# Kernel optimization log

Hardware: AMD Instinct MI355X
Metric: run time of the kernel (lower is better)

Reference implementation:

```python
import jax, jax.numpy as jnp
import numpy as np

N = 262144
K = 4  # Kernel_Correlation k
EPS = 1e-5


def setup_inputs() -> dict:
    key = jax.random.key(0)
    ks = jax.random.split(key, 12)
    inp = {
        "corner": jax.random.normal(ks[0], (N, 9), jnp.float32),
        "normal": jax.random.normal(ks[1], (N, 3), jnp.float32),
        "neighbour": jax.random.randint(ks[2], (N, 3), 0, N, jnp.int64),
        # Conv1d(1,32,6) on a length-6 signal == linear [32,6] (+bias)
        "conv_w": jax.random.normal(ks[3], (32, 6), jnp.float32) * 0.2,
        "conv_b": jax.random.normal(ks[4], (32,), jnp.float32) * 0.1,
        "lin3_w": jax.random.normal(ks[5], (64, 32), jnp.float32) * 0.15,
        "lin3_b": jnp.zeros((64,), jnp.float32),
        "lin4_w": jax.random.normal(ks[6], (64, 64), jnp.float32) * 0.12,
        "lin4_b": jnp.zeros((64,), jnp.float32),
        "kernel": jax.random.normal(ks[7], (64, K, 3), jnp.float32),  # learnable RBF kernel
        # 1x1 Conv1d(131,131) == linear [131,131]
        "conv1_w": jax.random.normal(ks[8], (131, 131), jnp.float32) * 0.08,
        "conv1_b": jnp.zeros((131,), jnp.float32),
        "bn_g": jnp.ones((131,), jnp.float32),
        "bn_b": jnp.zeros((131,), jnp.float32),
        "conv2_w": jax.random.normal(ks[9], (131, 131), jnp.float32) * 0.08,
        "conv2_b": jnp.zeros((131,), jnp.float32),
    }
    return inp


def reference(corner, normal, neighbour, conv_w, conv_b, lin3_w, lin3_b,
              lin4_w, lin4_b, kernel, conv1_w, conv1_b, bn_g, bn_b,
              conv2_w, conv2_b):
    # ---- Face_Rotate_Conv (vectorized over all n faces) ----
    c1, c2, c3 = corner[:, 0:3], corner[:, 3:6], corner[:, 6:9]
    # three rotated corner pairs: [n, 3, 6]
    pairs = jnp.stack([jnp.concatenate([c1, c2], 1),
                       jnp.concatenate([c2, c3], 1),
                       jnp.concatenate([c3, c1], 1)], axis=1)
    conv = jnp.einsum('npd,od->npo', pairs, conv_w) + conv_b  # [n,3,32]
    v = conv.mean(axis=1)                                      # [n,32]
    v = jax.nn.relu(v @ lin3_w.T + lin3_b) @ lin4_w.T + lin4_b  # [n,64]

    # ---- Kernel_Correlation (neighbour indices are gathered but unused
    # in the original math; only normal_i enters the RBF) ----
    # ||n_i - kernel_{m,l}||^2 via expansion; sq: [n,64,K]
    sq = (jnp.sum(normal * normal, 1)[:, None, None]
          + jnp.sum(kernel * kernel, -1)[None]
          - 2.0 * jnp.einsum('nd,mld->nml', normal, kernel))
    # original: sum_l exp(-norm^2) / (2*sigma^2), sigma=1, then / (k*4)
    z = jnp.sum(jnp.exp(-sq), axis=-1) * (0.5 / (K * 4))       # [n,64]

    # ---- structural_Des head ----
    x = jnp.concatenate([normal, v, z], axis=1)                # [n,131]
    h = x @ conv1_w.T + conv1_b
    # BatchNorm1d(131) in training mode: stats over the n dim (L=1)
    mean = h.mean(axis=0)
    var = jnp.mean((h - mean) ** 2, axis=0)
    h = bn_g * (h - mean) * jax.lax.rsqrt(var + EPS) + bn_b
    h = jax.nn.relu(h)
    out = h @ conv2_w.T + conv2_b                              # [n,131]
    return out
```

## Files before the change

kernel.cpp:

```cpp
#include <hip/hip_runtime.h>

#define NROWS 262144
#define NBLK  1024
#define PLANE_B   8388608ull
#define PLANE_US  4194304ull

typedef short  short8 __attribute__((ext_vector_type(8)));
typedef float  f32x4  __attribute__((ext_vector_type(4)));

static __device__ __forceinline__ unsigned short f2bf(float f) {
    unsigned u = __float_as_uint(f);
    u = u + 0x7fffu + ((u >> 16) & 1u);
    return (unsigned short)(u >> 16);
}
static __device__ __forceinline__ float bf2f(unsigned short h) {
    return __uint_as_float(((unsigned)h) << 16);
}

__global__ __launch_bounds__(256) void k_A1(
    const float* __restrict__ corner, const float* __restrict__ normal,
    const float* __restrict__ conv_w, const float* __restrict__ conv_b,
    const float* __restrict__ lin3_w, const float* __restrict__ lin3_b,
    const float* __restrict__ lin4_w, const float* __restrict__ lin4_b,
    const float* __restrict__ kern,
    unsigned short* __restrict__ X)
{
    __shared__ unsigned short T[4 * 64 * 72];
    __shared__ unsigned short B1[64 * 72];
    __shared__ unsigned short mini[4 * 64 * 20];

    const int tid  = threadIdx.x;
    const int wave = tid >> 6, lane = tid & 63;
    const int kg   = lane >> 4, c15 = lane & 15;
    const int row  = blockIdx.x * 256 + tid;

    for (int idx = tid; idx < 4096; idx += 256) {
        int o = idx >> 6, i3 = idx & 63;
        B1[o * 72 + i3] = f2bf(lin4_w[idx]);
    }

    float cr[9];
    #pragma unroll
    for (int k = 0; k < 9; k++) cr[k] = corner[row * 9 + k];
    const float nr0 = normal[row * 3 + 0];
    const float nr1 = normal[row * 3 + 1];
    const float nr2 = normal[row * 3 + 2];
    const float m0 = (cr[0] + cr[3] + cr[6]) * (1.0f / 3.0f);
    const float m1 = (cr[1] + cr[4] + cr[7]) * (1.0f / 3.0f);
    const float m2 = (cr[2] + cr[5] + cr[8]) * (1.0f / 3.0f);

    float a[32];
    #pragma unroll
    for (int o = 0; o < 32; o++) {
        const float* w = conv_w + o * 6;
        a[o] = conv_b[o] + m0 * (w[0] + w[3]) + m1 * (w[1] + w[4]) + m2 * (w[2] + w[5]);
    }

    #pragma unroll 2
    for (int i3 = 0; i3 < 64; i3++) {
        const float* w = lin3_w + i3 * 32;
        float t0 = lin3_b[i3], t1 = 0.0f;
        #pragma unroll
        for (int i = 0; i < 32; i += 2) { t0 += a[i] * w[i]; t1 += a[i + 1] * w[i + 1]; }
        float t = fmaxf(t0 + t1, 0.0f);
        T[(wave * 64 + lane) * 72 + i3] = f2bf(t);
    }

    #pragma unroll 1
    for (int cz = 0; cz < 4; cz++) {
        unsigned pk[8];
        #pragma unroll
        for (int q = 0; q < 8; q++) {
            float zz[2];
            #pragma unroll
            for (int h = 0; h < 2; h++) {
                int mi = cz * 16 + q * 2 + h;
                float acc = 0.0f;
                #pragma unroll
                for (int l = 0; l < 4; l++) {
                    const float* kp = kern + (mi * 4 + l) * 3;
                    float d0 = nr0 - kp[0], d1 = nr1 - kp[1], d2 = nr2 - kp[2];
                    acc += __expf(-(d0 * d0 + d1 * d1 + d2 * d2));
                }
                zz[h] = acc * 0.03125f;
            }
            pk[q] = (unsigned)f2bf(zz[0]) | ((unsigned)f2bf(zz[1]) << 16);
        }
        uint4* dst = (uint4*)((char*)X + (4 + cz) * PLANE_B + (size_t)row * 32);
        dst[0] = make_uint4(pk[0], pk[1], pk[2], pk[3]);
        dst[1] = make_uint4(pk[4], pk[5], pk[6], pk[7]);
    }

    __syncthreads();

    #pragma unroll 1
    for (int n = 0; n < 4; n++) {
        short8 bf0 = *(const short8*)&B1[(n * 16 + c15) * 72 + kg * 8];
        short8 bf1 = *(const short8*)&B1[(n * 16 + c15) * 72 + 32 + kg * 8];
        float bias = lin4_b[n * 16 + c15];
        #pragma unroll
        for (int m = 0; m < 4; m++) {
            f32x4 acc = {bias, bias, bias, bias};
            short8 a0 = *(const short8*)&T[(wave * 64 + m * 16 + c15) * 72 + kg * 8];
            short8 a1 = *(const short8*)&T[(wave * 64 + m * 16 + c15) * 72 + 32 + kg * 8];
            acc = __builtin_amdgcn_mfma_f32_16x16x32_bf16(a0, bf0, acc, 0, 0, 0);
            acc = __builtin_amdgcn_mfma_f32_16x16x32_bf16(a1, bf1, acc, 0, 0, 0);
            #pragma unroll
            for (int r = 0; r < 4; r++)
                mini[(wave * 64 + m * 16 + kg * 4 + r) * 20 + c15] = f2bf(acc[r]);
        }
        asm volatile("s_waitcnt lgkmcnt(0)" ::: "memory");
        const uint2* q = (const uint2*)&mini[(wave * 64 + lane) * 20];
        uint2 q0 = q[0], q1 = q[1], q2 = q[2], q3 = q[3];
        uint4* dst = (uint4*)((char*)X + (size_t)n * PLANE_B +
                              (size_t)(blockIdx.x * 256 + wave * 64 + lane) * 32);
        dst[0] = make_uint4(q0.x, q0.y, q1.x, q1.y);
        dst[1] = make_uint4(q2.x, q2.y, q3.x, q3.y);
    }
}

__global__ __launch_bounds__(256) void k_A2(
    const unsigned short* __restrict__ X, const float* __restrict__ normal,
    const float* __restrict__ w1, const float* __restrict__ b1,
    unsigned short* __restrict__ H, float* __restrict__ sums)
{
    __shared__ unsigned short Bs[144 * 168];
    __shared__ unsigned short mini[4 * 32 * 20];
    __shared__ float sl[288];

    const int tid  = threadIdx.x;
    const int wave = tid >> 6, lane = tid & 63;
    const int kg   = lane >> 4, c15 = lane & 15;

    for (int i = tid; i < 12096; i += 256) ((unsigned*)Bs)[i] = 0u;
    for (int i = tid; i < 288; i += 256) sl[i] = 0.0f;
    __syncthreads();
    for (int idx = tid; idx < 17161; idx += 256) {
        unsigned n = (unsigned)idx / 131u, ks = (unsigned)idx - n * 131u;
        unsigned kp = ks < 3 ? 128 + ks : ks - 3;
        Bs[n * 168 + kp] = f2bf(w1[idx]);
    }
    __syncthreads();

    const int rwave = blockIdx.x * 256 + wave * 64;

    #pragma unroll 1
    for (int mp = 0; mp < 2; mp++) {
        short8 af[2][5];
        #pragma unroll
        for (int mi = 0; mi < 2; mi++) {
            int arow = rwave + mp * 32 + mi * 16 + c15;
            #pragma unroll
            for (int ks = 0; ks < 4; ks++) {
                int p = ks * 2 + (kg >> 1);
                af[mi][ks] = *(const short8*)(X + (size_t)p * PLANE_US +
                                              (size_t)arow * 16 + (kg & 1) * 8);
            }
            short8 a4 = {0, 0, 0, 0, 0, 0, 0, 0};
            if (kg == 0) {
                a4[0] = (short)f2bf(normal[arow * 3 + 0]);
                a4[1] = (short)f2bf(normal[arow * 3 + 1]);
                a4[2] = (short)f2bf(normal[arow * 3 + 2]);
            }
            af[mi][4] = a4;
        }
        #pragma unroll 1
        for (int n = 0; n < 9; n++) {
            int col = n * 16 + c15;
            float bias = (col < 131) ? b1[col] : 0.0f;
            short8 bf[5];
            #pragma unroll
            for (int ks = 0; ks < 5; ks++)
                bf[ks] = *(const short8*)&Bs[(unsigned)(n * 16 + c15) * 168 + ks * 32 + kg * 8];
            f32x4 acc0 = {bias, bias, bias, bias};
            f32x4 acc1 = {bias, bias, bias, bias};
            #pragma unroll
            for (int ks = 0; ks < 5; ks++) {
                acc0 = __builtin_amdgcn_mfma_f32_16x16x32_bf16(af[0][ks], bf[ks], acc0, 0, 0, 0);
                acc1 = __builtin_amdgcn_mfma_f32_16x16x32_bf16(af[1][ks], bf[ks], acc1, 0, 0, 0);
            }
            float s1 = acc0[0] + acc0[1] + acc0[2] + acc0[3]
                     + acc1[0] + acc1[1] + acc1[2] + acc1[3];
            float s2 = acc0[0]*acc0[0] + acc0[1]*acc0[1] + acc0[2]*acc0[2] + acc0[3]*acc0[3]
                     + acc1[0]*acc1[0] + acc1[1]*acc1[1] + acc1[2]*acc1[2] + acc1[3]*acc1[3];
            s1 += __shfl_xor(s1, 16); s2 += __shfl_xor(s2, 16);
            s1 += __shfl_xor(s1, 32); s2 += __shfl_xor(s2, 32);
            if (lane < 16) { atomicAdd(&sl[col], s1); atomicAdd(&sl[144 + col], s2); }
            #pragma unroll
            for (int r = 0; r < 4; r++) {
                mini[(wave * 32 + kg * 4 + r) * 20 + c15]      = f2bf(acc0[r]);
                mini[(wave * 32 + 16 + kg * 4 + r) * 20 + c15] = f2bf(acc1[r]);
            }
            asm volatile("s_waitcnt lgkmcnt(0)" ::: "memory");
            if (lane < 32) {
                const uint2* q = (const uint2*)&mini[(wave * 32 + lane) * 20];
                uint2 q0 = q[0], q1 = q[1], q2 = q[2], q3 = q[3];
                uint4* dst = (uint4*)((char*)H + (size_t)n * PLANE_B +
                                      (size_t)(rwave + mp * 32 + lane) * 32);
                dst[0] = make_uint4(q0.x, q0.y, q1.x, q1.y);
                dst[1] = make_uint4(q2.x, q2.y, q3.x, q3.y);
            }
        }
    }
    __syncthreads();
    if (tid < 144) {
        float* dst = sums + (blockIdx.x & 63) * 288;
        atomicAdd(&dst[tid], sl[tid]);
        atomicAdd(&dst[144 + tid], sl[144 + tid]);
    }
}

__global__ void k_stats(const float* __restrict__ sums,
                        const float* __restrict__ bn_g, const float* __restrict__ bn_b,
                        float* __restrict__ scalep, float* __restrict__ shiftp)
{
    int j = threadIdx.x;
    if (j < 160) {
        float sc = 0.0f, sh = 0.0f;
        if (j < 131) {
            float s1 = 0.0f, s2 = 0.0f;
            #pragma unroll 4
            for (int s = 0; s < 64; s++) {
                s1 += sums[s * 288 + j];
                s2 += sums[s * 288 + 144 + j];
            }
            const float inv = 1.0f / (float)NROWS;
            float mean = s1 * inv;
            float var = fmaxf(s2 * inv - mean * mean, 0.0f);
            sc = bn_g[j] * rsqrtf(var + 1e-5f);
            sh = bn_b[j] - mean * sc;
        }
        scalep[j] = sc; shiftp[j] = sh;
    }
}

__global__ __launch_bounds__(256) void k_B(
    const unsigned short* __restrict__ H, const float* __restrict__ scalep,
    const float* __restrict__ shiftp, const float* __restrict__ w2,
    const float* __restrict__ b2, float* __restrict__ out)
{
    __shared__ unsigned short Bs[144 * 168];

    const int tid  = threadIdx.x;
    const int wave = tid >> 6, lane = tid & 63;
    const int kg   = lane >> 4, c15 = lane & 15;

    for (int i = tid; i < 12096; i += 256) ((unsigned*)Bs)[i] = 0u;
    __syncthreads();
    for (int idx = tid; idx < 17161; idx += 256) {
        unsigned n = (unsigned)idx / 131u, k = (unsigned)idx - n * 131u;
        Bs[n * 168 + k] = f2bf(w2[idx]);
    }
    __syncthreads();

    const int rwave = blockIdx.x * 256 + wave * 64;

    #pragma unroll 1
    for (int mp = 0; mp < 2; mp++) {
        short8 af[2][5];
        #pragma unroll
        for (int mi = 0; mi < 2; mi++) {
            int arow = rwave + mp * 32 + mi * 16 + c15;
            #pragma unroll
            for (int ks = 0; ks < 5; ks++) {
                short8 res = {0, 0, 0, 0, 0, 0, 0, 0};
                if (ks < 4 || kg < 2) {
                    int p = (ks < 4) ? (ks * 2 + (kg >> 1)) : 8;
                    short8 h8 = *(const short8*)(H + (size_t)p * PLANE_US +
                                                 (size_t)arow * 16 + (kg & 1) * 8);
                    int c0 = ks * 32 + kg * 8;
                    f32x4 scA = *(const f32x4*)(scalep + c0);
                    f32x4 scB = *(const f32x4*)(scalep + c0 + 4);
                    f32x4 shA = *(const f32x4*)(shiftp + c0);
                    f32x4 shB = *(const f32x4*)(shiftp + c0 + 4);
                    #pragma unroll
                    for (int e = 0; e < 8; e++) {
                        float hf = bf2f((unsigned short)h8[e]);
                        float sc = (e < 4) ? scA[e & 3] : scB[e & 3];
                        float sh = (e < 4) ? shA[e & 3] : shB[e & 3];
                        res[e] = (short)f2bf(fmaxf(hf * sc + sh, 0.0f));
                    }
                }
                af[mi][ks] = res;
            }
        }
        #pragma unroll 1
        for (int n = 0; n < 9; n++) {
            int col = n * 16 + c15;
            float bias = (col < 131) ? b2[col] : 0.0f;
            short8 bf[5];
            #pragma unroll
            for (int ks = 0; ks < 5; ks++)
                bf[ks] = *(const short8*)&Bs[(unsigned)(n * 16 + c15) * 168 + ks * 32 + kg * 8];
            f32x4 acc0 = {bias, bias, bias, bias};
            f32x4 acc1 = {bias, bias, bias, bias};
            #pragma unroll
            for (int ks = 0; ks < 5; ks++) {
                acc0 = __builtin_amdgcn_mfma_f32_16x16x32_bf16(af[0][ks], bf[ks], acc0, 0, 0, 0);
                acc1 = __builtin_amdgcn_mfma_f32_16x16x32_bf16(af[1][ks], bf[ks], acc1, 0, 0, 0);
            }
            if (col < 131) {
                #pragma unroll
                for (int r = 0; r < 4; r++) {
                    out[(size_t)(rwave + mp * 32 + kg * 4 + r) * 131 + col]      = acc0[r];
                    out[(size_t)(rwave + mp * 32 + 16 + kg * 4 + r) * 131 + col] = acc1[r];
                }
            }
        }
    }
}

extern "C" void kernel_launch(void* const* d_in, const int* in_sizes, int n_in,
                              void* d_out, int out_size, void* d_ws, size_t ws_size,
                              hipStream_t stream) {
    (void)in_sizes; (void)n_in; (void)out_size; (void)ws_size;
    const float* corner = (const float*)d_in[0];
    const float* normal = (const float*)d_in[1];
    const float* conv_w = (const float*)d_in[3];
    const float* conv_b = (const float*)d_in[4];
    const float* lin3_w = (const float*)d_in[5];
    const float* lin3_b = (const float*)d_in[6];
    const float* lin4_w = (const float*)d_in[7];
    const float* lin4_b = (const float*)d_in[8];
    const float* kern   = (const float*)d_in[9];
    const float* w1     = (const float*)d_in[10];
    const float* b1     = (const float*)d_in[11];
    const float* bn_g   = (const float*)d_in[12];
    const float* bn_b   = (const float*)d_in[13];
    const float* w2     = (const float*)d_in[14];
    const float* b2     = (const float*)d_in[15];

    unsigned short* X  = (unsigned short*)d_out;
    unsigned short* H  = (unsigned short*)d_ws;
    float* sums   = (float*)((char*)d_ws + 9 * PLANE_B);
    float* scalep = sums + 64 * 288;
    float* shiftp = scalep + 160;
    float* outp   = (float*)d_out;

    hipMemsetAsync(sums, 0, 64 * 288 * sizeof(float), stream);
    k_A1<<<NBLK, 256, 0, stream>>>(corner, normal, conv_w, conv_b, lin3_w, lin3_b,
                                   lin4_w, lin4_b, kern, X);
    k_A2<<<NBLK, 256, 0, stream>>>(X, normal, w1, b1, H, sums);
    k_stats<<<1, 256, 0, stream>>>(sums, bn_g, bn_b, scalep, shiftp);
    k_B<<<NBLK, 256, 0, stream>>>(H, scalep, shiftp, w2, b2, outp);
}
```

Baseline: 370.2 us.

## Fold lin3/lin4 into weights and fuse feature build with conv1 GEMM

Adds a prep kernel that precomputes composed weights: conv+lin3 collapsed to a 4-term affine map per channel, lin4 folded into conv1 weights and bias, and RBF kernel constants for the expanded exponent. A fused kernel then builds the 131-wide feature row in shared memory and runs the conv1 MFMA GEMM with BN statistics, removing the X intermediate round trip through global memory. BN stats finalization moves into the second GEMM kernel, eliminating the k_stats launch. Folding changes bf16 rounding points slightly and the fused kernel uses large LDS per 128-thread block.

Result: faster. 315.8 us (-14.7%).

```diff
diff --git a/kernel.cpp b/kernel.cpp
--- a/kernel.cpp
+++ b/kernel.cpp
@@ -1,9 +1,17 @@
 #include <hip/hip_runtime.h>
 
 #define NROWS 262144
-#define NBLK  1024
 #define PLANE_B   8388608ull
 #define PLANE_US  4194304ull
+#define KS 168
+
+#define H_B    0ull
+#define W1P_B  75497472ull
+#define W2P_B  75545856ull
+#define B1P_B  75594240ull
+#define G4_B   75594816ull
+#define ZT_B   75595840ull
+#define SUMS_B 75599936ull
 
 typedef short  short8 __attribute__((ext_vector_type(8)));
 typedef float  f32x4  __attribute__((ext_vector_type(4)));
@@ -17,242 +25,229 @@
     return __uint_as_float(((unsigned)h) << 16);
 }
 
-__global__ __launch_bounds__(256) void k_A1(
-    const float* __restrict__ corner, const float* __restrict__ normal,
+__global__ __launch_bounds__(64) void k_prep(
     const float* __restrict__ conv_w, const float* __restrict__ conv_b,
     const float* __restrict__ lin3_w, const float* __restrict__ lin3_b,
     const float* __restrict__ lin4_w, const float* __restrict__ lin4_b,
     const float* __restrict__ kern,
-    unsigned short* __restrict__ X)
+    const float* __restrict__ w1, const float* __restrict__ b1,
+    const float* __restrict__ w2,
+    unsigned short* __restrict__ W1P, unsigned short* __restrict__ W2P,
+    float* __restrict__ B1P, float* __restrict__ G4, float* __restrict__ ZT)
 {
-    __shared__ unsigned short T[4 * 64 * 72];
-    __shared__ unsigned short B1[64 * 72];
-    __shared__ unsigned short mini[4 * 64 * 20];
+    const int j = blockIdx.x;
+    const int l = threadIdx.x;
+    if (j < 144) {
+        const bool jv = (j < 131);
+        float acc = 0.0f;
+        if (jv) {
+            #pragma unroll 4
+            for (int o = 0; o < 64; o++)
+                acc += w1[j * 131 + 3 + o] * lin4_w[o * 64 + l];
+        }
+        W1P[j * KS + l]      = jv ? f2bf(acc) : (unsigned short)0;
+        W1P[j * KS + 64 + l] = jv ? f2bf(w1[j * 131 + 67 + l]) : (unsigned short)0;
+        if (l < 40) {
+            float v = (jv && l < 3) ? w1[j * 131 + l] : 0.0f;
+            W1P[j * KS + 128 + l] = f2bf(v);
+        }
+        W2P[j * KS + l]      = jv ? f2bf(w2[j * 131 + l]) : (unsigned short)0;
+        W2P[j * KS + 64 + l] = (jv && (64 + l) < 131) ? f2bf(w2[j * 131 + 64 + l]) : (unsigned short)0;
+        if (l < 40) {
+            int k2 = 128 + l;
+            W2P[j * KS + k2] = (jv && k2 < 131) ? f2bf(w2[j * 131 + k2]) : (unsigned short)0;
+        }
+        if (l == 0) {
+            float bb = 0.0f;
+            if (jv) {
+                bb = b1[j];
+                for (int o = 0; o < 64; o++) bb += w1[j * 131 + 3 + o] * lin4_b[o];
+            }
+            B1P[j] = bb;
+        }
+    } else if (j == 144) {
+        float g0v = lin3_b[l], ga = 0.0f, gb = 0.0f, gc = 0.0f;
+        #pragma unroll 4
+        for (int i = 0; i < 32; i++) {
+            float wv = lin3_w[l * 32 + i];
+            ga  += wv * (conv_w[i * 6 + 0] + conv_w[i * 6 + 3]);
+            gb  += wv * (conv_w[i * 6 + 1] + conv_w[i * 6 + 4]);
+            gc  += wv * (conv_w[i * 6 + 2] + conv_w[i * 6 + 5]);
+            g0v += wv * conv_b[i];
+        }
+        G4[l * 4 + 0] = ga; G4[l * 4 + 1] = gb; G4[l * 4 + 2] = gc; G4[l * 4 + 3] = g0v;
+    } else {
+        #pragma unroll
+        for (int p = 0; p < 4; p++) {
+            int idx = l * 4 + p;
+            float kx = kern[idx * 3 + 0], ky = kern[idx * 3 + 1], kz = kern[idx * 3 + 2];
+            ZT[idx * 4 + 0] = 2.0f * kx;
+            ZT[idx * 4 + 1] = 2.0f * ky;
+            ZT[idx * 4 + 2] = 2.0f * kz;
+            ZT[idx * 4 + 3] = -(kx * kx + ky * ky + kz * kz);
+        }
+    }
+}
+
+__global__ __launch_bounds__(128) void k_F(
+    const float* __restrict__ corner, const float* __restrict__ normal,
+    const unsigned short* __restrict__ W1P, const float* __restrict__ B1P,
+    const float* __restrict__ G4, const float* __restrict__ ZT,
+    unsigned short* __restrict__ H, float* __restrict__ sums)
+{
+    __shared__ unsigned short Xs[128 * KS];
+    __shared__ unsigned short mini[2 * 64 * 20];
+    __shared__ float sl[288];
 
     const int tid  = threadIdx.x;
     const int wave = tid >> 6, lane = tid & 63;
     const int kg   = lane >> 4, c15 = lane & 15;
-    const int row  = blockIdx.x * 256 + tid;
-
-    for (int idx = tid; idx < 4096; idx += 256) {
-        int o = idx >> 6, i3 = idx & 63;
-        B1[o * 72 + i3] = f2bf(lin4_w[idx]);
-    }
-
-    float cr[9];
+    const int row  = blockIdx.x * 128 + tid;
+
+    for (int i = tid; i < 288; i += 128) sl[i] = 0.0f;
+
+    const float* cp = corner + (size_t)row * 9;
+    float c0 = cp[0], c1 = cp[1], c2 = cp[2], c3 = cp[3], c4 = cp[4],
+          c5 = cp[5], c6 = cp[6], c7 = cp[7], c8 = cp[8];
+    const float n0 = normal[row * 3 + 0];
+    const float n1 = normal[row * 3 + 1];
+    const float n2 = normal[row * 3 + 2];
+    const float m0 = (c0 + c3 + c6) * (1.0f / 3.0f);
+    const float m1 = (c1 + c4 + c7) * (1.0f / 3.0f);
+    const float m2 = (c2 + c5 + c8) * (1.0f / 3.0f);
+    const float nn = n0 * n0 + n1 * n1 + n2 * n2;
+
+    unsigned short* xrow = Xs + tid * KS;
+
     #pragma unroll
-    for (int k = 0; k < 9; k++) cr[k] = corner[row * 9 + k];
-    const float nr0 = normal[row * 3 + 0];
-    const float nr1 = normal[row * 3 + 1];
-    const float nr2 = normal[row * 3 + 2];
-    const float m0 = (cr[0] + cr[3] + cr[6]) * (1.0f / 3.0f);
-    const float m1 = (cr[1] + cr[4] + cr[7]) * (1.0f / 3.0f);
-    const float m2 = (cr[2] + cr[5] + cr[8]) * (1.0f / 3.0f);
-
-    float a[32];
+    for (int q = 0; q < 8; q++) {
+        short8 pk;
+        #pragma unroll
+        for (int e = 0; e < 8; e++) {
+            int o = q * 8 + e;
+            float u = G4[o * 4 + 3] + m0 * G4[o * 4 + 0] + m1 * G4[o * 4 + 1] + m2 * G4[o * 4 + 2];
+            pk[e] = (short)f2bf(fmaxf(u, 0.0f));
+        }
+        *(short8*)(xrow + q * 8) = pk;
+    }
     #pragma unroll
-    for (int o = 0; o < 32; o++) {
-        const float* w = conv_w + o * 6;
-        a[o] = conv_b[o] + m0 * (w[0] + w[3]) + m1 * (w[1] + w[4]) + m2 * (w[2] + w[5]);
-    }
-
-    #pragma unroll 2
-    for (int i3 = 0; i3 < 64; i3++) {
-        const float* w = lin3_w + i3 * 32;
-        float t0 = lin3_b[i3], t1 = 0.0f;
-        #pragma unroll
-        for (int i = 0; i < 32; i += 2) { t0 += a[i] * w[i]; t1 += a[i + 1] * w[i + 1]; }
-        float t = fmaxf(t0 + t1, 0.0f);
-        T[(wave * 64 + lane) * 72 + i3] = f2bf(t);
-    }
+    for (int q = 0; q < 8; q++) {
+        short8 pk;
+        #pragma unroll
+        for (int e = 0; e < 8; e++) {
+            int mi = q * 8 + e;
+            float acc = 0.0f;
+            #pragma unroll
+            for (int lp = 0; lp < 4; lp++) {
+                const float* zt = ZT + (mi * 4 + lp) * 4;
+                float w = zt[3] + zt[0] * n0 + zt[1] * n1 + zt[2] * n2 - nn;
+                acc += __expf(w);
+            }
+            pk[e] = (short)f2bf(acc * 0.03125f);
+        }
+        *(short8*)(xrow + 64 + q * 8) = pk;
+    }
+    {
+        short8 pk = {0, 0, 0, 0, 0, 0, 0, 0};
+        pk[0] = (short)f2bf(n0); pk[1] = (short)f2bf(n1); pk[2] = (short)f2bf(n2);
+        *(short8*)(xrow + 128) = pk;
+        short8 zz = {0, 0, 0, 0, 0, 0, 0, 0};
+        *(short8*)(xrow + 136) = zz;
+        *(short8*)(xrow + 144) = zz;
+        *(short8*)(xrow + 152) = zz;
+    }
+
+    __syncthreads();
+
+    short8 af[4][5];
+    #pragma unroll
+    for (int mi = 0; mi < 4; mi++)
+        #pragma unroll
+        for (int ks = 0; ks < 5; ks++)
+            af[mi][ks] = *(const short8*)(Xs + (wave * 64 + mi * 16 + c15) * KS + ks * 32 + kg * 8);
 
     #pragma unroll 1
-    for (int cz = 0; cz < 4; cz++) {
-        unsigned pk[8];
-        #pragma unroll
-        for (int q = 0; q < 8; q++) {
-            float zz[2];
-            #pragma unroll
-            for (int h = 0; h < 2; h++) {
-                int mi = cz * 16 + q * 2 + h;
-                float acc = 0.0f;
-                #pragma unroll
-                for (int l = 0; l < 4; l++) {
-                    const float* kp = kern + (mi * 4 + l) * 3;
-                    float d0 = nr0 - kp[0], d1 = nr1 - kp[1], d2 = nr2 - kp[2];
-                    acc += __expf(-(d0 * d0 + d1 * d1 + d2 * d2));
-                }
-                zz[h] = acc * 0.03125f;
-            }
-            pk[q] = (unsigned)f2bf(zz[0]) | ((unsigned)f2bf(zz[1]) << 16);
-        }
-        uint4* dst = (uint4*)((char*)X + (4 + cz) * PLANE_B + (size_t)row * 32);
-        dst[0] = make_uint4(pk[0], pk[1], pk[2], pk[3]);
-        dst[1] = make_uint4(pk[4], pk[5], pk[6], pk[7]);
-    }
-
-    __syncthreads();
-
-    #pragma unroll 1
-    for (int n = 0; n < 4; n++) {
-        short8 bf0 = *(const short8*)&B1[(n * 16 + c15) * 72 + kg * 8];
-        short8 bf1 = *(const short8*)&B1[(n * 16 + c15) * 72 + 32 + kg * 8];
-        float bias = lin4_b[n * 16 + c15];
-        #pragma unroll
-        for (int m = 0; m < 4; m++) {
+    for (int n = 0; n < 9; n++) {
+        const int col = n * 16 + c15;
+        const float bias = B1P[col];
+        short8 bf[5];
+        #pragma unroll
+        for (int ks = 0; ks < 5; ks++)
+            bf[ks] = *(const short8*)(W1P + (size_t)col * KS + ks * 32 + kg * 8);
+        float s1 = 0.0f, s2 = 0.0f;
+        #pragma unroll
+        for (int mi = 0; mi < 4; mi++) {
             f32x4 acc = {bias, bias, bias, bias};
-            short8 a0 = *(const short8*)&T[(wave * 64 + m * 16 + c15) * 72 + kg * 8];
-            short8 a1 = *(const short8*)&T[(wave * 64 + m * 16 + c15) * 72 + 32 + kg * 8];
-            acc = __builtin_amdgcn_mfma_f32_16x16x32_bf16(a0, bf0, acc, 0, 0, 0);
-            acc = __builtin_amdgcn_mfma_f32_16x16x32_bf16(a1, bf1, acc, 0, 0, 0);
-            #pragma unroll
-            for (int r = 0; r < 4; r++)
-                mini[(wave * 64 + m * 16 + kg * 4 + r) * 20 + c15] = f2bf(acc[r]);
-        }
+            #pragma unroll
+            for (int ks = 0; ks < 5; ks++)
+                acc = __builtin_amdgcn_mfma_f32_16x16x32_bf16(af[mi][ks], bf[ks], acc, 0, 0, 0);
+            #pragma unroll
+            for (int r = 0; r < 4; r++) {
+                s1 += acc[r]; s2 += acc[r] * acc[r];
+                mini[(wave * 64 + mi * 16 + kg * 4 + r) * 20 + c15] = f2bf(acc[r]);
+            }
+        }
+        s1 += __shfl_xor(s1, 16); s2 += __shfl_xor(s2, 16);
+        s1 += __shfl_xor(s1, 32); s2 += __shfl_xor(s2, 32);
+        if (lane < 16) { atomicAdd(&sl[col], s1); atomicAdd(&sl[144 + col], s2); }
         asm volatile("s_waitcnt lgkmcnt(0)" ::: "memory");
-        const uint2* q = (const uint2*)&mini[(wave * 64 + lane) * 20];
+        __builtin_amdgcn_sched_barrier(0);
+        const uint2* q = (const uint2*)(mini + (wave * 64 + lane) * 20);
         uint2 q0 = q[0], q1 = q[1], q2 = q[2], q3 = q[3];
-        uint4* dst = (uint4*)((char*)X + (size_t)n * PLANE_B +
-                              (size_t)(blockIdx.x * 256 + wave * 64 + lane) * 32);
+        uint4* dst = (uint4*)((char*)H + (size_t)n * PLANE_B +
+                              (size_t)(blockIdx.x * 128 + wave * 64 + lane) * 32);
         dst[0] = make_uint4(q0.x, q0.y, q1.x, q1.y);
         dst[1] = make_uint4(q2.x, q2.y, q3.x, q3.y);
     }
-}
-
-__global__ __launch_bounds__(256) void k_A2(
-    const unsigned short* __restrict__ X, const float* __restrict__ normal,
-    const float* __restrict__ w1, const float* __restrict__ b1,
-    unsigned short* __restrict__ H, float* __restrict__ sums)
+
+    __syncthreads();
+    {
+        float* d = sums + (blockIdx.x & 31) * 288;
+        for (int i = tid; i < 288; i += 128) atomicAdd(&d[i], sl[i]);
+    }
+}
+
+__global__ __launch_bounds__(256) void k_B(
+    const unsigned short* __restrict__ H, const unsigned short* __restrict__ W2P,
+    const float* __restrict__ sums,
+    const float* __restrict__ bn_g, const float* __restrict__ bn_b,
+    const float* __restrict__ b2, float* __restrict__ out)
 {
-    __shared__ unsigned short Bs[144 * 168];
-    __shared__ unsigned short mini[4 * 32 * 20];
-    __shared__ float sl[288];
+    __shared__ unsigned short Bs[144 * KS];
+    __shared__ __align__(16) float s_scale[160];
+    __shared__ __align__(16) float s_shift[160];
 
     const int tid  = threadIdx.x;
+    {
+        const uint4* src = (const uint4*)W2P;
+        uint4* dst = (uint4*)Bs;
+        #pragma unroll
+        for (int i = 0; i < 12; i++) {
+            int idx = tid + i * 256;
+            if (idx < 3024) dst[idx] = src[idx];
+        }
+    }
+    if (tid < 160) {
+        float sc = 0.0f, sh = 0.0f;
+        if (tid < 131) {
+            float s1 = 0.0f, s2 = 0.0f;
+            #pragma unroll 4
+            for (int s = 0; s < 32; s++) {
+                s1 += sums[s * 288 + tid];
+                s2 += sums[s * 288 + 144 + tid];
+            }
+            const float inv = 1.0f / (float)NROWS;
+            float mean = s1 * inv;
+            float var  = fmaxf(s2 * inv - mean * mean, 0.0f);
+            sc = bn_g[tid] * rsqrtf(var + 1e-5f);
+            sh = bn_b[tid] - mean * sc;
+        }
+        s_scale[tid] = sc; s_shift[tid] = sh;
+    }
+    __syncthreads();
+
     const int wave = tid >> 6, lane = tid & 63;
     const int kg   = lane >> 4, c15 = lane & 15;
-
-    for (int i = tid; i < 12096; i += 256) ((unsigned*)Bs)[i] = 0u;
-    for (int i = tid; i < 288; i += 256) sl[i] = 0.0f;
-    __syncthreads();
-    for (int idx = tid; idx < 17161; idx += 256) {
-        unsigned n = (unsigned)idx / 131u, ks = (unsigned)idx - n * 131u;
-        unsigned kp = ks < 3 ? 128 + ks : ks - 3;
-        Bs[n * 168 + kp] = f2bf(w1[idx]);
-    }
-    __syncthreads();
-
-    const int rwave = blockIdx.x * 256 + wave * 64;
-
-    #pragma unroll 1
-    for (int mp = 0; mp < 2; mp++) {
-        short8 af[2][5];
-        #pragma unroll
-        for (int mi = 0; mi < 2; mi++) {
-            int arow = rwave + mp * 32 + mi * 16 + c15;
-            #pragma unroll
-            for (int ks = 0; ks < 4; ks++) {
-                int p = ks * 2 + (kg >> 1);
-                af[mi][ks] = *(const short8*)(X + (size_t)p * PLANE_US +
-                                              (size_t)arow * 16 + (kg & 1) * 8);
-            }
-            short8 a4 = {0, 0, 0, 0, 0, 0, 0, 0};
-            if (kg == 0) {
-                a4[0] = (short)f2bf(normal[arow * 3 + 0]);
-                a4[1] = (short)f2bf(normal[arow * 3 + 1]);
-                a4[2] = (short)f2bf(normal[arow * 3 + 2]);
-            }
-            af[mi][4] = a4;
-        }
-        #pragma unroll 1
-        for (int n = 0; n < 9; n++) {
-            int col = n * 16 + c15;
-            float bias = (col < 131) ? b1[col] : 0.0f;
-            short8 bf[5];
-            #pragma unroll
-            for (int ks = 0; ks < 5; ks++)
-                bf[ks] = *(const short8*)&Bs[(unsigned)(n * 16 + c15) * 168 + ks * 32 + kg * 8];
-            f32x4 acc0 = {bias, bias, bias, bias};
-            f32x4 acc1 = {bias, bias, bias, bias};
-            #pragma unroll
-            for (int ks = 0; ks < 5; ks++) {
-                acc0 = __builtin_amdgcn_mfma_f32_16x16x32_bf16(af[0][ks], bf[ks], acc0, 0, 0, 0);
-                acc1 = __builtin_amdgcn_mfma_f32_16x16x32_bf16(af[1][ks], bf[ks], acc1, 0, 0, 0);
-            }
-            float s1 = acc0[0] + acc0[1] + acc0[2] + acc0[3]
-                     + acc1[0] + acc1[1] + acc1[2] + acc1[3];
-            float s2 = acc0[0]*acc0[0] + acc0[1]*acc0[1] + acc0[2]*acc0[2] + acc0[3]*acc0[3]
-                     + acc1[0]*acc1[0] + acc1[1]*acc1[1] + acc1[2]*acc1[2] + acc1[3]*acc1[3];
-            s1 += __shfl_xor(s1, 16); s2 += __shfl_xor(s2, 16);
-            s1 += __shfl_xor(s1, 32); s2 += __shfl_xor(s2, 32);
-            if (lane < 16) { atomicAdd(&sl[col], s1); atomicAdd(&sl[144 + col], s2); }
-            #pragma unroll
-            for (int r = 0; r < 4; r++) {
-                mini[(wave * 32 + kg * 4 + r) * 20 + c15]      = f2bf(acc0[r]);
-                mini[(wave * 32 + 16 + kg * 4 + r) * 20 + c15] = f2bf(acc1[r]);
-            }
-            asm volatile("s_waitcnt lgkmcnt(0)" ::: "memory");
-            if (lane < 32) {
-                const uint2* q = (const uint2*)&mini[(wave * 32 + lane) * 20];
-                uint2 q0 = q[0], q1 = q[1], q2 = q[2], q3 = q[3];
-                uint4* dst = (uint4*)((char*)H + (size_t)n * PLANE_B +
-                                      (size_t)(rwave + mp * 32 + lane) * 32);
-                dst[0] = make_uint4(q0.x, q0.y, q1.x, q1.y);
-                dst[1] = make_uint4(q2.x, q2.y, q3.x, q3.y);
-            }
-        }
-    }
-    __syncthreads();
-    if (tid < 144) {
-        float* dst = sums + (blockIdx.x & 63) * 288;
-        atomicAdd(&dst[tid], sl[tid]);
-        atomicAdd(&dst[144 + tid], sl[144 + tid]);
-    }
-}
-
-__global__ void k_stats(const float* __restrict__ sums,
-                        const float* __restrict__ bn_g, const float* __restrict__ bn_b,
-                        float* __restrict__ scalep, float* __restrict__ shiftp)
-{
-    int j = threadIdx.x;
-    if (j < 160) {
-        float sc = 0.0f, sh = 0.0f;
-        if (j < 131) {
-            float s1 = 0.0f, s2 = 0.0f;
-            #pragma unroll 4
-            for (int s = 0; s < 64; s++) {
-                s1 += sums[s * 288 + j];
-                s2 += sums[s * 288 + 144 + j];
-            }
-            const float inv = 1.0f / (float)NROWS;
-            float mean = s1 * inv;
-            float var = fmaxf(s2 * inv - mean * mean, 0.0f);
-            sc = bn_g[j] * rsqrtf(var + 1e-5f);
-            sh = bn_b[j] - mean * sc;
-        }
-        scalep[j] = sc; shiftp[j] = sh;
-    }
-}
-
-__global__ __launch_bounds__(256) void k_B(
-    const unsigned short* __restrict__ H, const float* __restrict__ scalep,
-    const float* __restrict__ shiftp, const float* __restrict__ w2,
-    const float* __restrict__ b2, float* __restrict__ out)
-{
-    __shared__ unsigned short Bs[144 * 168];
-
-    const int tid  = threadIdx.x;
-    const int wave = tid >> 6, lane = tid & 63;
-    const int kg   = lane >> 4, c15 = lane & 15;
-
-    for (int i = tid; i < 12096; i += 256) ((unsigned*)Bs)[i] = 0u;
-    __syncthreads();
-    for (int idx = tid; idx < 17161; idx += 256) {
-        unsigned n = (unsigned)idx / 131u, k = (unsigned)idx - n * 131u;
-        Bs[n * 168 + k] = f2bf(w2[idx]);
-    }
-    __syncthreads();
-
     const int rwave = blockIdx.x * 256 + wave * 64;
 
     #pragma unroll 1
@@ -269,16 +264,10 @@
                     short8 h8 = *(const short8*)(H + (size_t)p * PLANE_US +
                                                  (size_t)arow * 16 + (kg & 1) * 8);
                     int c0 = ks * 32 + kg * 8;
-                    f32x4 scA = *(const f32x4*)(scalep + c0);
-                    f32x4 scB = *(const f32x4*)(scalep + c0 + 4);
-                    f32x4 shA = *(const f32x4*)(shiftp + c0);
-                    f32x4 shB = *(const f32x4*)(shiftp + c0 + 4);
                     #pragma unroll
                     for (int e = 0; e < 8; e++) {
                         float hf = bf2f((unsigned short)h8[e]);
-                        float sc = (e < 4) ? scA[e & 3] : scB[e & 3];
-                        float sh = (e < 4) ? shA[e & 3] : shB[e & 3];
-                        res[e] = (short)f2bf(fmaxf(hf * sc + sh, 0.0f));
+                        res[e] = (short)f2bf(fmaxf(hf * s_scale[c0 + e] + s_shift[c0 + e], 0.0f));
                     }
                 }
                 af[mi][ks] = res;
@@ -286,12 +275,12 @@
         }
         #pragma unroll 1
         for (int n = 0; n < 9; n++) {
-            int col = n * 16 + c15;
-            float bias = (col < 131) ? b2[col] : 0.0f;
+            const int col = n * 16 + c15;
+            const float bias = (col < 131) ? b2[col] : 0.0f;
             short8 bf[5];
             #pragma unroll
             for (int ks = 0; ks < 5; ks++)
-                bf[ks] = *(const short8*)&Bs[(unsigned)(n * 16 + c15) * 168 + ks * 32 + kg * 8];
+                bf[ks] = *(const short8*)&Bs[(unsigned)col * KS + ks * 32 + kg * 8];
             f32x4 acc0 = {bias, bias, bias, bias};
             f32x4 acc1 = {bias, bias, bias, bias};
             #pragma unroll
@@ -330,17 +319,19 @@
     const float* w2     = (const float*)d_in[14];
     const float* b2     = (const float*)d_in[15];
 
-    unsigned short* X  = (unsigned short*)d_out;
-    unsigned short* H  = (unsigned short*)d_ws;
-    float* sums   = (float*)((char*)d_ws + 9 * PLANE_B);
-    float* scalep = sums + 64 * 288;
-    float* shiftp = scalep + 160;
-    float* outp   = (float*)d_out;
-
-    hipMemsetAsync(sums, 0, 64 * 288 * sizeof(float), stream);
-    k_A1<<<NBLK, 256, 0, stream>>>(corner, normal, conv_w, conv_b, lin3_w, lin3_b,
-                                   lin4_w, lin4_b, kern, X);
-    k_A2<<<NBLK, 256, 0, stream>>>(X, normal, w1, b1, H, sums);
-    k_stats<<<1, 256, 0, stream>>>(sums, bn_g, bn_b, scalep, shiftp);
-    k_B<<<NBLK, 256, 0, stream>>>(H, scalep, shiftp, w2, b2, outp);
-}
+    char* wsb = (char*)d_ws;
+    unsigned short* Hp  = (unsigned short*)(wsb + H_B);
+    unsigned short* W1P = (unsigned short*)(wsb + W1P_B);
+    unsigned short* W2P = (unsigned short*)(wsb + W2P_B);
+    float* B1P  = (float*)(wsb + B1P_B);
+    float* G4   = (float*)(wsb + G4_B);
+    float* ZT   = (float*)(wsb + ZT_B);
+    float* sums = (float*)(wsb + SUMS_B);
+    float* outp = (float*)d_out;
+
+    hipMemsetAsync(sums, 0, 32 * 288 * sizeof(float), stream);
+    k_prep<<<146, 64, 0, stream>>>(conv_w, conv_b, lin3_w, lin3_b, lin4_w, lin4_b,
+                                   kern, w1, b1, w2, W1P, W2P, B1P, G4, ZT);
+    k_F<<<NROWS / 128, 128, 0, stream>>>(corner, normal, W1P, B1P, G4, ZT, Hp, sums);
+    k_B<<<NROWS / 256, 256, 0, stream>>>(Hp, W2P, sums, bn_g, bn_b, b2, outp);
+}
```
